# Optimization experiments

Measured on AMD Instinct MI355X. Metric: run time of the kernel, lower is better.

The kernel has to match this reference:

```python
import jax, jax.numpy as jnp
import numpy as np

N, T = 8192, 8192
RB, CB = 64, 64  # row_blocks, col_blocks
HID = 3          # hidden_upper from mar_small_config


def _partition_ids(total, nblocks, rng):
    # mirrors: ones + multinomial(remaining), every block >= 1
    part = np.ones(nblocks, dtype=np.int64)
    part += rng.multinomial(total - nblocks, [1.0 / nblocks] * nblocks)
    return np.repeat(np.arange(nblocks), part).astype(np.int32)


def setup_inputs() -> dict:
    key = jax.random.key(0)
    ks = jax.random.split(key, 4)
    rng = np.random.default_rng(42)
    X = jax.random.normal(ks[0], (N, T), dtype=jnp.float32)
    row_ids = jnp.asarray(_partition_ids(N, RB, rng))  # [N] sorted block ids
    col_ids = jnp.asarray(_partition_ids(T, CB, rng))  # [T] sorted block ids
    W1 = jax.random.normal(ks[1], (1, HID), dtype=jnp.float32)
    b1 = jnp.zeros((HID,), jnp.float32)
    W2 = jax.random.normal(ks[2], (HID, HID), dtype=jnp.float32)
    b2 = jnp.zeros((HID,), jnp.float32)
    W3 = jax.random.normal(ks[3], (HID, 1), dtype=jnp.float32)
    b3 = jnp.zeros((1,), jnp.float32)
    return {"X": X, "row_ids": row_ids, "col_ids": col_ids,
            "W1": W1, "b1": b1, "W2": W2, "b2": b2, "W3": W3, "b3": b3}


def _block_mean(X, row_ids, col_ids):
    # fused segment-reduce replacing the O(RB*CB) python loop + .item() syncs
    row_counts = jax.ops.segment_sum(jnp.ones((N,), X.dtype), row_ids, num_segments=RB)
    col_counts = jax.ops.segment_sum(jnp.ones((T,), X.dtype), col_ids, num_segments=CB)
    s = jax.ops.segment_sum(X, row_ids, num_segments=RB)        # [RB, T]
    s = jax.ops.segment_sum(s.T, col_ids, num_segments=CB).T    # [RB, CB]
    return s / (row_counts[:, None] * col_counts[None, :]), row_counts, col_counts


def _mar_generator(x_small, W1, b1, W2, b2, W3, b3):
    # small per-cell relu MLP -> sigmoid propensity (stand-in for MAR_missingness)
    h = x_small[..., None]                    # [RB, CB, 1]
    h = jax.nn.relu(h @ W1 + b1)
    h = jax.nn.relu(h @ W2 + b2)
    return jax.nn.sigmoid((h @ W3 + b3)[..., 0])  # [RB, CB]


def reference(X, row_ids, col_ids, W1, b1, W2, b2, W3, b3):
    x_small, row_counts, col_counts = _block_mean(X, row_ids, col_ids)
    propensity = _mar_generator(x_small, W1, b1, W2, b2, W3, b3)
    row_cumsum = jnp.concatenate([jnp.zeros((1,), jnp.int32),
                                  jnp.cumsum(row_counts.astype(jnp.int32))])
    col_cumsum = jnp.concatenate([jnp.zeros((1,), jnp.int32),
                                  jnp.cumsum(col_counts.astype(jnp.int32))])
    return propensity, row_cumsum, col_cumsum
```

## Files before the change

### kernel.cpp

```cpp
#include <hip/hip_runtime.h>
#include <math.h>

#define NROWS 8192
#define NCOLS 8192
#define RB 64
#define CB 64

__global__ __launch_bounds__(256) void block_rowsum_kernel(
    const float* __restrict__ X,
    const int*   __restrict__ row_ids,
    float*       __restrict__ s1)
{
    __shared__ int rids[64];
    const int tid = threadIdx.x;
    const int r0  = blockIdx.y * 64;
    const int c   = blockIdx.x * 1024 + tid * 4;

    if (tid < 64) rids[tid] = row_ids[r0 + tid];
    __syncthreads();

    float4 acc = make_float4(0.f, 0.f, 0.f, 0.f);
    int cur = rids[0];
    const float* Xp = X + (size_t)r0 * NCOLS + c;

    #pragma unroll 4
    for (int i = 0; i < 64; ++i) {
        const int rb = rids[i];
        if (rb != cur) {
            float* d = s1 + (size_t)cur * NCOLS + c;
            atomicAdd(d + 0, acc.x); atomicAdd(d + 1, acc.y);
            atomicAdd(d + 2, acc.z); atomicAdd(d + 3, acc.w);
            acc = make_float4(0.f, 0.f, 0.f, 0.f);
            cur = rb;
        }
        const float4 v = *(const float4*)(Xp + (size_t)i * NCOLS);
        acc.x += v.x; acc.y += v.y; acc.z += v.z; acc.w += v.w;
    }
    float* d = s1 + (size_t)cur * NCOLS + c;
    atomicAdd(d + 0, acc.x); atomicAdd(d + 1, acc.y);
    atomicAdd(d + 2, acc.z); atomicAdd(d + 3, acc.w);
}

__global__ __launch_bounds__(256) void counts_kernel(
    const int* __restrict__ row_ids,
    const int* __restrict__ col_ids,
    float*     __restrict__ out,
    float*     __restrict__ cnts)
{
    __shared__ int cnt[64];
    const int tid = threadIdx.x;
    const int* ids = (blockIdx.x == 0) ? row_ids : col_ids;
    const int n = (blockIdx.x == 0) ? NROWS : NCOLS;

    if (tid < 64) cnt[tid] = 0;
    __syncthreads();
    for (int i = tid; i < n; i += blockDim.x)
        atomicAdd(&cnt[ids[i]], 1);
    __syncthreads();

    if (tid < 64) cnts[blockIdx.x * 64 + tid] = (float)cnt[tid];
    if (tid == 0) {
        float* obase = out + RB * CB + blockIdx.x * (RB + 1);
        int c = 0;
        obase[0] = 0.0f;
        for (int i = 0; i < 64; ++i) { c += cnt[i]; obase[i + 1] = (float)c; }
    }
}

__global__ __launch_bounds__(256) void colreduce_mlp_kernel(
    const float* __restrict__ s1,
    const int*   __restrict__ col_ids,
    const float* __restrict__ cnts,
    const float* __restrict__ W1, const float* __restrict__ b1,
    const float* __restrict__ W2, const float* __restrict__ b2,
    const float* __restrict__ W3, const float* __restrict__ b3,
    float*       __restrict__ out)
{
    __shared__ float acc[64];
    const int tid = threadIdx.x;
    const int rb  = blockIdx.x;

    if (tid < 64) acc[tid] = 0.0f;
    __syncthreads();

    const int c0 = tid * 32;
    const float* sp = s1 + (size_t)rb * NCOLS + c0;
    int cur = col_ids[c0];
    float s = 0.f;
    for (int j = 0; j < 32; ++j) {
        const int cb = col_ids[c0 + j];
        if (cb != cur) { atomicAdd(&acc[cur], s); s = 0.f; cur = cb; }
        s += sp[j];
    }
    atomicAdd(&acc[cur], s);
    __syncthreads();

    if (tid < 64) {
        const int cb = tid;
        const float mean = acc[cb] / (cnts[rb] * cnts[64 + cb]);

        float h1[3], h2[3];
        #pragma unroll
        for (int j = 0; j < 3; ++j)
            h1[j] = fmaxf(mean * W1[j] + b1[j], 0.f);
        #pragma unroll
        for (int j = 0; j < 3; ++j) {
            float v = b2[j];
            #pragma unroll
            for (int i = 0; i < 3; ++i) v += h1[i] * W2[i * 3 + j];
            h2[j] = fmaxf(v, 0.f);
        }
        float z = b3[0];
        #pragma unroll
        for (int i = 0; i < 3; ++i) z += h2[i] * W3[i];

        out[rb * 64 + cb] = 1.0f / (1.0f + expf(-z));
    }
}

extern "C" void kernel_launch(void* const* d_in, const int* in_sizes, int n_in,
                              void* d_out, int out_size, void* d_ws, size_t ws_size,
                              hipStream_t stream) {
    const float* X       = (const float*)d_in[0];
    const int*   row_ids = (const int*)  d_in[1];
    const int*   col_ids = (const int*)  d_in[2];
    const float* W1      = (const float*)d_in[3];
    const float* b1      = (const float*)d_in[4];
    const float* W2      = (const float*)d_in[5];
    const float* b2      = (const float*)d_in[6];
    const float* W3      = (const float*)d_in[7];
    const float* b3      = (const float*)d_in[8];
    float* out = (float*)d_out;

    float* s1   = (float*)d_ws;
    float* cnts = s1 + (size_t)RB * NCOLS;

    hipMemsetAsync(d_ws, 0, (size_t)RB * NCOLS * sizeof(float), stream);

    counts_kernel<<<2, 256, 0, stream>>>(row_ids, col_ids, out, cnts);
    block_rowsum_kernel<<<dim3(8, 128), 256, 0, stream>>>(X, row_ids, s1);
    colreduce_mlp_kernel<<<64, 256, 0, stream>>>(s1, col_ids, cnts,
                                                 W1, b1, W2, b2, W3, b3, out);
}
```

Before: 403.4 us.

## Fuse column reduction into row-block sum via shared-memory histogram atomics

```diff
diff --git a/kernel.cpp b/kernel.cpp
--- a/kernel.cpp
+++ b/kernel.cpp
@@ -6,116 +6,109 @@
 #define RB 64
 #define CB 64
 
-__global__ __launch_bounds__(256) void block_rowsum_kernel(
+__global__ __launch_bounds__(256) void fused_blocksum_kernel(
     const float* __restrict__ X,
     const int*   __restrict__ row_ids,
-    float*       __restrict__ s1)
+    const int*   __restrict__ col_ids,
+    float*       __restrict__ acc_g,
+    float*       __restrict__ cnts,
+    float*       __restrict__ out)
 {
-    __shared__ int rids[64];
+    __shared__ int   rids[64];
+    __shared__ float lacc[64];
+    __shared__ int   hist[64];
+
     const int tid = threadIdx.x;
-    const int r0  = blockIdx.y * 64;
-    const int c   = blockIdx.x * 1024 + tid * 4;
+    const int bx  = blockIdx.x & 7;
+    const int by  = blockIdx.x >> 3;
 
-    if (tid < 64) rids[tid] = row_ids[r0 + tid];
+    if (blockIdx.x < 2) {
+        const int* ids = (blockIdx.x == 0) ? row_ids : col_ids;
+        if (tid < 64) hist[tid] = 0;
+        __syncthreads();
+        for (int i = tid; i < NROWS; i += 256)
+            atomicAdd(&hist[ids[i]], 1);
+        __syncthreads();
+        if (tid < 64) cnts[blockIdx.x * 64 + tid] = (float)hist[tid];
+        if (tid == 0) {
+            float* obase = out + RB * CB + blockIdx.x * (RB + 1);
+            int c = 0;
+            obase[0] = 0.0f;
+            for (int i = 0; i < 64; ++i) { c += hist[i]; obase[i + 1] = (float)c; }
+        }
+        __syncthreads();
+    }
+
+    if (tid < 64) {
+        rids[tid] = row_ids[by * 64 + tid];
+        lacc[tid] = 0.0f;
+    }
     __syncthreads();
 
-    float4 acc = make_float4(0.f, 0.f, 0.f, 0.f);
+    const int c = bx * 1024 + tid * 4;
+    const int4 cb4 = *(const int4*)(col_ids + c);
+    const float* Xp = X + (size_t)by * 64 * NCOLS + c;
+
+    float4 a = make_float4(0.f, 0.f, 0.f, 0.f);
     int cur = rids[0];
-    const float* Xp = X + (size_t)r0 * NCOLS + c;
 
     #pragma unroll 4
     for (int i = 0; i < 64; ++i) {
         const int rb = rids[i];
         if (rb != cur) {
-            float* d = s1 + (size_t)cur * NCOLS + c;
-            atomicAdd(d + 0, acc.x); atomicAdd(d + 1, acc.y);
-            atomicAdd(d + 2, acc.z); atomicAdd(d + 3, acc.w);
-            acc = make_float4(0.f, 0.f, 0.f, 0.f);
+            atomicAdd(&lacc[cb4.x], a.x);
+            atomicAdd(&lacc[cb4.y], a.y);
+            atomicAdd(&lacc[cb4.z], a.z);
+            atomicAdd(&lacc[cb4.w], a.w);
+            __syncthreads();
+            if (tid < 64 && lacc[tid] != 0.0f)
+                atomicAdd(&acc_g[cur * 64 + tid], lacc[tid]);
+            __syncthreads();
+            if (tid < 64) lacc[tid] = 0.0f;
+            __syncthreads();
+            a = make_float4(0.f, 0.f, 0.f, 0.f);
             cur = rb;
         }
         const float4 v = *(const float4*)(Xp + (size_t)i * NCOLS);
-        acc.x += v.x; acc.y += v.y; acc.z += v.z; acc.w += v.w;
+        a.x += v.x; a.y += v.y; a.z += v.z; a.w += v.w;
     }
-    float* d = s1 + (size_t)cur * NCOLS + c;
-    atomicAdd(d + 0, acc.x); atomicAdd(d + 1, acc.y);
-    atomicAdd(d + 2, acc.z); atomicAdd(d + 3, acc.w);
+    atomicAdd(&lacc[cb4.x], a.x);
+    atomicAdd(&lacc[cb4.y], a.y);
+    atomicAdd(&lacc[cb4.z], a.z);
+    atomicAdd(&lacc[cb4.w], a.w);
+    __syncthreads();
+    if (tid < 64 && lacc[tid] != 0.0f)
+        atomicAdd(&acc_g[cur * 64 + tid], lacc[tid]);
 }
 
-__global__ __launch_bounds__(256) void counts_kernel(
-    const int* __restrict__ row_ids,
-    const int* __restrict__ col_ids,
-    float*     __restrict__ out,
-    float*     __restrict__ cnts)
-{
-    __shared__ int cnt[64];
-    const int tid = threadIdx.x;
-    const int* ids = (blockIdx.x == 0) ? row_ids : col_ids;
-    const int n = (blockIdx.x == 0) ? NROWS : NCOLS;
-
-    if (tid < 64) cnt[tid] = 0;
-    __syncthreads();
-    for (int i = tid; i < n; i += blockDim.x)
-        atomicAdd(&cnt[ids[i]], 1);
-    __syncthreads();
-
-    if (tid < 64) cnts[blockIdx.x * 64 + tid] = (float)cnt[tid];
-    if (tid == 0) {
-        float* obase = out + RB * CB + blockIdx.x * (RB + 1);
-        int c = 0;
-        obase[0] = 0.0f;
-        for (int i = 0; i < 64; ++i) { c += cnt[i]; obase[i + 1] = (float)c; }
-    }
-}
-
-__global__ __launch_bounds__(256) void colreduce_mlp_kernel(
-    const float* __restrict__ s1,
-    const int*   __restrict__ col_ids,
+__global__ __launch_bounds__(256) void mlp_kernel(
+    const float* __restrict__ acc_g,
     const float* __restrict__ cnts,
     const float* __restrict__ W1, const float* __restrict__ b1,
     const float* __restrict__ W2, const float* __restrict__ b2,
     const float* __restrict__ W3, const float* __restrict__ b3,
     float*       __restrict__ out)
 {
-    __shared__ float acc[64];
-    const int tid = threadIdx.x;
-    const int rb  = blockIdx.x;
+    const int cell = blockIdx.x * 256 + threadIdx.x;
+    const int rb = cell >> 6, cb = cell & 63;
+    const float mean = acc_g[cell] / (cnts[rb] * cnts[64 + cb]);
 
-    if (tid < 64) acc[tid] = 0.0f;
-    __syncthreads();
+    float h1[3], h2[3];
+    #pragma unroll
+    for (int j = 0; j < 3; ++j)
+        h1[j] = fmaxf(mean * W1[j] + b1[j], 0.f);
+    #pragma unroll
+    for (int j = 0; j < 3; ++j) {
+        float v = b2[j];
+        #pragma unroll
+        for (int i = 0; i < 3; ++i) v += h1[i] * W2[i * 3 + j];
+        h2[j] = fmaxf(v, 0.f);
+    }
+    float z = b3[0];
+    #pragma unroll
+    for (int i = 0; i < 3; ++i) z += h2[i] * W3[i];
 
-    const int c0 = tid * 32;
-    const float* sp = s1 + (size_t)rb * NCOLS + c0;
-    int cur = col_ids[c0];
-    float s = 0.f;
-    for (int j = 0; j < 32; ++j) {
-        const int cb = col_ids[c0 + j];
-        if (cb != cur) { atomicAdd(&acc[cur], s); s = 0.f; cur = cb; }
-        s += sp[j];
-    }
-    atomicAdd(&acc[cur], s);
-    __syncthreads();
-
-    if (tid < 64) {
-        const int cb = tid;
-        const float mean = acc[cb] / (cnts[rb] * cnts[64 + cb]);
-
-        float h1[3], h2[3];
-        #pragma unroll
-        for (int j = 0; j < 3; ++j)
-            h1[j] = fmaxf(mean * W1[j] + b1[j], 0.f);
-        #pragma unroll
-        for (int j = 0; j < 3; ++j) {
-            float v = b2[j];
-            #pragma unroll
-            for (int i = 0; i < 3; ++i) v += h1[i] * W2[i * 3 + j];
-            h2[j] = fmaxf(v, 0.f);
-        }
-        float z = b3[0];
-        #pragma unroll
-        for (int i = 0; i < 3; ++i) z += h2[i] * W3[i];
-
-        out[rb * 64 + cb] = 1.0f / (1.0f + expf(-z));
-    }
+    out[cell] = 1.0f / (1.0f + expf(-z));
 }
 
 extern "C" void kernel_launch(void* const* d_in, const int* in_sizes, int n_in,
@@ -132,13 +125,13 @@
     const float* b3      = (const float*)d_in[8];
     float* out = (float*)d_out;
 
-    float* s1   = (float*)d_ws;
-    float* cnts = s1 + (size_t)RB * NCOLS;
+    float* acc_g = (float*)d_ws;
+    float* cnts  = acc_g + RB * CB;
 
-    hipMemsetAsync(d_ws, 0, (size_t)RB * NCOLS * sizeof(float), stream);
+    hipMemsetAsync(d_ws, 0, (RB * CB + 128) * sizeof(float), stream);
 
-    counts_kernel<<<2, 256, 0, stream>>>(row_ids, col_ids, out, cnts);
-    block_rowsum_kernel<<<dim3(8, 128), 256, 0, stream>>>(X, row_ids, s1);
-    colreduce_mlp_kernel<<<64, 256, 0, stream>>>(s1, col_ids, cnts,
-                                                 W1, b1, W2, b2, W3, b3, out);
+    fused_blocksum_kernel<<<1024, 256, 0, stream>>>(X, row_ids, col_ids,
+                                                    acc_g, cnts, out);
+    mlp_kernel<<<16, 256, 0, stream>>>(acc_g, cnts,
+                                       W1, b1, W2, b2, W3, b3, out);
 }
```

Result: faster. 387.3 us (-4.0%).
